# Performance work log

Measured on AMD Instinct MI355X. Metric: run time of the kernel, lower is better.

## Reference

```python
import jax, jax.numpy as jnp
import numpy as np

NUM_SCALE_LAYERS = [16, 8, 8]
B, H, N = 32, 512, 64
NUM_PROPS = 2080


def _pool_specs():
    # (kernel, stride) per layer, matching the torch ModuleList construction
    specs = []
    for scale_idx, num_layer in enumerate(NUM_SCALE_LAYERS):
        first = (1, 1) if scale_idx == 0 else (3, 2)
        specs.append([first] + [(2, 1)] * (num_layer - 1))
    return specs


def _maxpool1d(x, k, s):
    # x: [B, H, L] -> valid max pool along last axis
    return jax.lax.reduce_window(x, -jnp.inf, jax.lax.max,
                                 (1, 1, k), (1, 1, s), 'VALID')


def setup_inputs() -> dict:
    key = jax.random.key(0)
    kx, ks, ke = jax.random.split(key, 3)
    x = jax.random.normal(kx, (B, H, N), dtype=jnp.float32)
    starts = jax.random.randint(ks, (NUM_PROPS,), 0, N)          # props[:,0] in [0, N)
    ends = jax.random.randint(ke, (NUM_PROPS,), 1, N + 1)        # props[:,1] in [1, N]
    props = jnp.stack([starts, ends], axis=1).astype(jnp.int64)
    return {"x": x, "props": props}


def reference(x, props):
    batch_size, hidden_size, ori_num_clips = x.shape
    ori_map_h = jnp.zeros((batch_size, hidden_size, ori_num_clips, ori_num_clips), x.dtype)
    ori_map_mask = jnp.zeros((batch_size, 1, ori_num_clips, ori_num_clips), x.dtype)
    acum_layers = 0
    stride = 1
    for scale_layers in _pool_specs():
        for i, (k, s) in enumerate(scale_layers):
            stride = stride * s
            x = _maxpool1d(x, k, s)
            # static (trace-time) diagonal index lists, exactly as the torch code
            s_idxs = np.arange(0, ori_num_clips - acum_layers - i * stride, stride)
            e_idxs = s_idxs + acum_layers + i * stride
            ori_map_h = ori_map_h.at[:, :, s_idxs, e_idxs].set(x)
            ori_map_mask = ori_map_mask.at[:, :, s_idxs, e_idxs].set(1.0)
        acum_layers += stride * (len(scale_layers) + 1)
    props_h = ori_map_h[:, :, props[:, 0], props[:, 1] - 1]      # [B, H, P]
    ori_map_mask = ori_map_mask.at[:, :, props[:, 0], props[:, 1] - 1].set(1.0)
    return props_h.swapaxes(1, 2), ori_map_h, ori_map_mask
```

## Files before the change

kernel.cpp:

```cpp
#include <hip/hip_runtime.h>
#include <math.h>

#define PB 32
#define PH 512
#define PN 64
#define PP 2080

#define OFF_MAP  ((size_t)PB * PP * PH)
#define OFF_MASK (OFF_MAP + (size_t)PB * PH * PN * PN)

__device__ __forceinline__ bool pair_valid(int s, int e) {
    int d = e - s;
    if (d < 0) return false;
    if (d <= 15) return true;
    if (d <= 31) return (d & 1) && !(s & 1);
    return d >= 35 && ((d & 3) == 3) && !(s & 3);
}

#define K2_LVL 2112
#define K2_ZROW 12672
#define LDS_FLOATS 12706

#define K1_ROWS 8
#define K1_RS 392
#define K1_ZERO 390

#define GRID_BLOCKS 2592

__global__ __launch_bounds__(256) void fused_kernel(const float* __restrict__ x,
                                                    const int* __restrict__ props,
                                                    float* __restrict__ out) {
    __shared__ float Lf[LDS_FLOATS];
    const int tid = threadIdx.x;
    const int g = blockIdx.x;

    if (g < 2560) {
        const int q = g / 5;
        const int r = g - q * 5;
        if (r != 0) {
            const int kb = q * 4 + (r - 1);
            const size_t rowBase = (size_t)kb * K1_ROWS;
            const int wave = tid >> 6;
            const int lane = tid & 63;

            int a1[16], a2[16];
#pragma unroll
            for (int i = 0; i < 16; ++i) {
                const int s = wave * 16 + i;
                const int e = lane;
                const bool good = pair_valid(s, e);
                const int k = good ? min(31 - __clz(e - s + 1), 5) : 0;
                a1[i] = good ? 65 * k + s : K1_ZERO;
                a2[i] = good ? 65 * k + (e + 1 - (1 << k)) : K1_ZERO;
            }

#pragma unroll
            for (int i = tid; i < K1_ROWS * 64; i += 256) {
                const int rr = i >> 6, c = i & 63;
                Lf[rr * K1_RS + c] = x[rowBase * 64 + i];
            }
            if (tid < K1_ROWS) Lf[tid * K1_RS + K1_ZERO] = 0.0f;
            __syncthreads();

#pragma unroll
            for (int k = 1; k <= 5; ++k) {
                const int off = 1 << (k - 1);
#pragma unroll
                for (int i = tid; i < K1_ROWS * 64; i += 256) {
                    const int rr = i >> 6, c = i & 63;
                    const float* Lp = Lf + rr * K1_RS + 65 * (k - 1);
                    Lf[rr * K1_RS + 65 * k + c] = fmaxf(Lp[c], Lp[min(c + off, 63)]);
                }
                __syncthreads();
            }

#pragma unroll 2
            for (int rr = 0; rr < K1_ROWS; ++rr) {
                const float* Lr = Lf + rr * K1_RS;
                float* orow = out + OFF_MAP + (rowBase + rr) * 4096 + lane;
#pragma unroll
                for (int i = 0; i < 16; ++i) {
                    orow[(wave * 16 + i) * 64] = fmaxf(Lr[a1[i]], Lr[a2[i]]);
                }
            }
        } else {
            const int b  = q >> 4;
            const int h0 = (q & 15) * 32;

            const float* xb = x + ((size_t)b * PH + h0) * PN;
#pragma unroll
            for (int i = tid; i < 32 * 64; i += 256) {
                const int h = i >> 6, n = i & 63;
                Lf[n * 33 + h] = xb[i];
            }
            if (tid < 33) Lf[K2_ZROW + tid] = 0.0f;
            __syncthreads();

#pragma unroll 1
            for (int k = 1; k <= 5; ++k) {
                const int off = 1 << (k - 1);
#pragma unroll
                for (int i = tid; i < 64 * 32; i += 256) {
                    const int n = i >> 5, h = i & 31;
                    const float* Lp = Lf + (k - 1) * K2_LVL;
                    Lf[k * K2_LVL + n * 33 + h] =
                        fmaxf(Lp[n * 33 + h], Lp[min(n + off, 63) * 33 + h]);
                }
                __syncthreads();
            }

            const int wave = tid >> 6;
            const int sub  = (tid >> 5) & 1;
            const int h    = tid & 31;
            const int2* props2 = (const int2*)props;
            float* ob = out + (size_t)b * PP * PH + h0 + h;
#pragma unroll 4
            for (int i = 0; i < PP / 8; ++i) {
                const int idx = i * 8 + wave * 2 + sub;
                const int2 pr = props2[idx];
                const int s = pr.x, e1 = pr.y - 1;
                const bool good = pair_valid(s, e1);
                const int k = good ? min(31 - __clz(e1 - s + 1), 5) : 0;
                const int A1 = good ? k * K2_LVL + s * 33 : K2_ZROW;
                const int A2 = good ? k * K2_LVL + (e1 + 1 - (1 << k)) * 33 : K2_ZROW;
                ob[(size_t)idx * PH] = fmaxf(Lf[A1 + h], Lf[A2 + h]);
            }
        }
    } else {
        const int b = g - 2560;

        for (int i = tid; i < 4096; i += 256)
            Lf[i] = pair_valid(i >> 6, i & 63) ? 1.0f : 0.0f;
        __syncthreads();

        for (int p = tid; p < PP; p += 256) {
            const int2 pr = ((const int2*)props)[p];
            Lf[pr.x * 64 + (pr.y - 1)] = 1.0f;
        }
        __syncthreads();

        float4* ob = (float4*)(out + OFF_MASK + (size_t)b * 4096);
        const float4* lb = (const float4*)Lf;
#pragma unroll
        for (int i = tid; i < 1024; i += 256)
            ob[i] = lb[i];
    }
}

extern "C" void kernel_launch(void* const* d_in, const int* in_sizes, int n_in,
                              void* d_out, int out_size, void* d_ws, size_t ws_size,
                              hipStream_t stream) {
    const float* x = (const float*)d_in[0];
    const int* props = (const int*)d_in[1];
    float* out = (float*)d_out;

    fused_kernel<<<GRID_BLOCKS, 256, 0, stream>>>(x, props, out);
}
```

Baseline: 440.1 us.

## Split proposal gather across more blocks with precomputed LDS address table

The proposal-gather work is split four ways across props, giving 2048 gather blocks interleaved with the 2048 map blocks instead of the old 1:4 ratio. Each gather block precomputes its per-proposal sparse-table LDS offsets into shared memory once, instead of decoding props in the hot loop. The sparse-table levels are stored compactly so only valid entries are built, which shrinks the LDS footprint. The cost is that each gather block now rebuilds the full pooling table from x, so that work is repeated four times as often.

```diff
diff --git a/kernel.cpp b/kernel.cpp
--- a/kernel.cpp
+++ b/kernel.cpp
@@ -17,28 +17,28 @@
     return d >= 35 && ((d & 3) == 3) && !(s & 3);
 }
 
-#define K2_LVL 2112
-#define K2_ZROW 12672
-#define LDS_FLOATS 12706
+
+#define K2_ZSLOT 10791
+#define K2_ADDR  10824
+#define LDS_FLOATS 11864
 
 #define K1_ROWS 8
 #define K1_RS 392
 #define K1_ZERO 390
 
-#define GRID_BLOCKS 2592
+#define GRID_BLOCKS 4128
 
 __global__ __launch_bounds__(256) void fused_kernel(const float* __restrict__ x,
                                                     const int* __restrict__ props,
                                                     float* __restrict__ out) {
     __shared__ float Lf[LDS_FLOATS];
+    int* Li = (int*)Lf;
     const int tid = threadIdx.x;
     const int g = blockIdx.x;
 
-    if (g < 2560) {
-        const int q = g / 5;
-        const int r = g - q * 5;
-        if (r != 0) {
-            const int kb = q * 4 + (r - 1);
+    if (g < 4096) {
+        if (!(g & 1)) {
+            const int kb = g >> 1;
             const size_t rowBase = (size_t)kb * K1_ROWS;
             const int wave = tid >> 6;
             const int lane = tid & 63;
@@ -84,8 +84,10 @@
                 }
             }
         } else {
-            const int b  = q >> 4;
-            const int h0 = (q & 15) * 32;
+            const int j  = g >> 1;
+            const int b  = j >> 6;
+            const int h0 = ((j >> 2) & 15) * 32;
+            const int p0 = (j & 3) * 520;
 
             const float* xb = x + ((size_t)b * PH + h0) * PN;
 #pragma unroll
@@ -93,18 +95,29 @@
                 const int h = i >> 6, n = i & 63;
                 Lf[n * 33 + h] = xb[i];
             }
-            if (tid < 33) Lf[K2_ZROW + tid] = 0.0f;
+            if (tid < 33) Lf[K2_ZSLOT + tid] = 0.0f;
+
+            for (int t = tid; t < 520; t += 256) {
+                const int2 pr = ((const int2*)props)[p0 + t];
+                const int s = pr.x, e1 = pr.y - 1;
+                const bool good = pair_valid(s, e1);
+                const int k = good ? min(31 - __clz(e1 - s + 1), 5) : 0;
+                const int base = 65 * k - (1 << k) + 1;
+                Li[K2_ADDR + 2 * t]     = good ? (base + s) * 33 : K2_ZSLOT;
+                Li[K2_ADDR + 2 * t + 1] = good ? (base + e1 + 1 - (1 << k)) * 33 : K2_ZSLOT;
+            }
             __syncthreads();
 
 #pragma unroll 1
             for (int k = 1; k <= 5; ++k) {
-                const int off = 1 << (k - 1);
-#pragma unroll
-                for (int i = tid; i < 64 * 32; i += 256) {
+                const int off   = 1 << (k - 1);
+                const int bcur  = 65 * k - (1 << k) + 1;
+                const int bprev = 65 * (k - 1) - off + 1;
+                const int cnt   = 65 - (1 << k);
+                for (int i = tid; i < cnt * 32; i += 256) {
                     const int n = i >> 5, h = i & 31;
-                    const float* Lp = Lf + (k - 1) * K2_LVL;
-                    Lf[k * K2_LVL + n * 33 + h] =
-                        fmaxf(Lp[n * 33 + h], Lp[min(n + off, 63) * 33 + h]);
+                    Lf[(bcur + n) * 33 + h] =
+                        fmaxf(Lf[(bprev + n) * 33 + h], Lf[(bprev + n + off) * 33 + h]);
                 }
                 __syncthreads();
             }
@@ -112,22 +125,17 @@
             const int wave = tid >> 6;
             const int sub  = (tid >> 5) & 1;
             const int h    = tid & 31;
-            const int2* props2 = (const int2*)props;
             float* ob = out + (size_t)b * PP * PH + h0 + h;
 #pragma unroll 4
-            for (int i = 0; i < PP / 8; ++i) {
+            for (int i = 0; i < 65; ++i) {
                 const int idx = i * 8 + wave * 2 + sub;
-                const int2 pr = props2[idx];
-                const int s = pr.x, e1 = pr.y - 1;
-                const bool good = pair_valid(s, e1);
-                const int k = good ? min(31 - __clz(e1 - s + 1), 5) : 0;
-                const int A1 = good ? k * K2_LVL + s * 33 : K2_ZROW;
-                const int A2 = good ? k * K2_LVL + (e1 + 1 - (1 << k)) * 33 : K2_ZROW;
-                ob[(size_t)idx * PH] = fmaxf(Lf[A1 + h], Lf[A2 + h]);
+                const int2 aa = *(const int2*)&Li[K2_ADDR + 2 * idx];
+                const float v = fmaxf(Lf[aa.x + h], Lf[aa.y + h]);
+                ob[(size_t)(p0 + idx) * PH] = v;
             }
         }
     } else {
-        const int b = g - 2560;
+        const int b = g - 4096;
 
         for (int i = tid; i < 4096; i += 256)
             Lf[i] = pair_valid(i >> 6, i & 63) ? 1.0f : 0.0f;
```

Result: faster. 405.0 us (-8.0%).
